# Optimization experiments

Hardware: AMD Instinct MI355X
Metric: run time of the kernel (lower is better)

## Reference

```python
import jax, jax.numpy as jnp
import numpy as np
from jax import lax

WS = 8      # window size (square)
SS = 4      # shift size
HEADS = 8
K = 9       # snake-conv kernel size
CENTER = K // 2
EXT = 1.0   # extend_scope


def _shift_attn_mask(H, W):
    # static numpy construction of Swin shift mask -> [num_windows, L, L]
    m = np.zeros((H, W), dtype=np.float32)
    cnt = 0
    for hs in [(0, -WS), (-WS, -SS), (-SS, None)]:
        for ws_ in [(0, -WS), (-WS, -SS), (-SS, None)]:
            m[hs[0]:hs[1], ws_[0]:ws_[1]] = cnt
            cnt += 1
    m = m.reshape(H // WS, WS, W // WS, WS).transpose(0, 2, 1, 3).reshape(-1, WS * WS)
    d = m[:, None, :] - m[:, :, None]
    return jnp.asarray(np.where(d != 0, -100.0, 0.0).astype(np.float32))


def shifted_window_attention(x, qkv_w, qkv_b, proj_w, proj_b, rel_bias):
    B, H, W, C = x.shape
    d = C // HEADS
    x = jnp.roll(x, shift=(-SS, -SS), axis=(1, 2))
    nH, nW = H // WS, W // WS
    nwin, L = nH * nW, WS * WS
    # window partition -> [B*nwin, L, C]
    xw = x.reshape(B, nH, WS, nW, WS, C).transpose(0, 1, 3, 2, 4, 5).reshape(B * nwin, L, C)
    qkv = (xw @ qkv_w.T + qkv_b).reshape(B * nwin, L, 3, HEADS, d).transpose(2, 0, 3, 1, 4)
    q, k, v = qkv[0] * (d ** -0.5), qkv[1], qkv[2]
    attn = jnp.einsum('nhld,nhmd->nhlm', q, k) + rel_bias[None]
    amask = _shift_attn_mask(H, W)  # [nwin, L, L]
    attn = attn.reshape(B, nwin, HEADS, L, L) + amask[None, :, None]
    attn = jax.nn.softmax(attn.reshape(B * nwin, HEADS, L, L), axis=-1)
    out = jnp.einsum('nhlm,nhmd->nhld', attn, v).transpose(0, 2, 1, 3).reshape(B * nwin, L, C)
    out = out @ proj_w.T + proj_b
    out = out.reshape(B, nH, nW, WS, WS, C).transpose(0, 1, 3, 2, 4, 5).reshape(B, H, W, C)
    return jnp.roll(out, shift=(SS, SS), axis=(1, 2))


def snake_coordinate_map(offset):
    # offset [B, 2K, Wd, Hd], morph=0: cumulative y offsets from the kernel center
    B, _, Wd, Hd = offset.shape
    y_off = offset[:, :K]
    # y_new[center]=0; y_new[center+i]=sum_{j=1..i} y_off[center+j]; mirror below
    up = jnp.cumsum(y_off[:, CENTER + 1:], axis=1)
    down = jnp.cumsum(y_off[:, :CENTER][:, ::-1], axis=1)[:, ::-1]
    y_cum = jnp.concatenate([down, jnp.zeros((B, 1, Wd, Hd), offset.dtype), up], axis=1)
    y_center = jnp.arange(Wd, dtype=offset.dtype)[None, None, :, None]
    y_new = y_center + EXT * y_cum                              # [B,K,Wd,Hd]
    x_spread = jnp.linspace(-CENTER, CENTER, K, dtype=offset.dtype)[None, :, None, None]
    x_center = jnp.arange(Hd, dtype=offset.dtype)[None, None, None, :]
    x_new = jnp.broadcast_to(x_center + x_spread, (B, K, Wd, Hd))
    # rearrange 'b k w h -> b (w k) h'
    y_map = y_new.transpose(0, 2, 1, 3).reshape(B, Wd * K, Hd)
    x_map = x_new.transpose(0, 2, 1, 3).reshape(B, Wd * K, Hd)
    return y_map, x_map


def bilinear_sample(feat, ymap, xmap):
    Hin, Win = feat.shape[-2], feat.shape[-1]
    y = jnp.clip(ymap, 0.0, Hin - 1.0)
    x = jnp.clip(xmap, 0.0, Win - 1.0)
    y0f, x0f = jnp.floor(y), jnp.floor(x)
    wy, wx = y - y0f, x - x0f
    y0 = y0f.astype(jnp.int32); x0 = x0f.astype(jnp.int32)
    y1 = jnp.minimum(y0 + 1, Hin - 1); x1 = jnp.minimum(x0 + 1, Win - 1)
    g = jax.vmap(lambda f, yy, xx: f[:, yy, xx])  # -> [B,C,Ho,Wo]
    v00 = g(feat, y0, x0); v01 = g(feat, y0, x1)
    v10 = g(feat, y1, x0); v11 = g(feat, y1, x1)
    wy = wy[:, None]; wx = wx[:, None]
    return v00 * (1 - wy) * (1 - wx) + v01 * (1 - wy) * wx + v10 * wy * (1 - wx) + v11 * wy * wx


def _forward(x, qkv_weight, qkv_bias, proj_weight, proj_bias, rel_bias, offset, dsc_weight, dsc_bias):
    y = shifted_window_attention(x, qkv_weight, qkv_bias, proj_weight, proj_bias, rel_bias)
    feat = y.transpose(0, 3, 1, 2)                      # NCHW
    ymap, xmap = snake_coordinate_map(offset)
    samp = bilinear_sample(feat, ymap, xmap)            # [B,C,H*K,W]
    out = lax.conv_general_dilated(samp, dsc_weight, window_strides=(K, 1), padding='VALID',
                                   dimension_numbers=('NCHW', 'OIHW', 'NCHW'))
    return jax.nn.relu(out + dsc_bias[None, :, None, None])


def setup_inputs() -> dict:
    key = jax.random.key(0)
    ks = jax.random.split(key, 9)
    B, H, W, C = 8, 64, 64, 256
    return {
        'x': jax.random.normal(ks[0], (B, H, W, C), jnp.float32),
        'qkv_weight': jax.random.normal(ks[1], (3 * C, C), jnp.float32) * 0.05,
        'qkv_bias': jax.random.normal(ks[2], (3 * C,), jnp.float32) * 0.05,
        'proj_weight': jax.random.normal(ks[3], (C, C), jnp.float32) * 0.05,
        'proj_bias': jax.random.normal(ks[4], (C,), jnp.float32) * 0.05,
        'rel_bias': jax.random.normal(ks[5], (HEADS, WS * WS, WS * WS), jnp.float32) * 0.05,
        'offset': jax.random.normal(ks[6], (B, 2 * K, H, W), jnp.float32),
        'dsc_weight': jax.random.normal(ks[7], (C, C, K, 1), jnp.float32) * 0.02,
        'dsc_bias': jax.random.normal(ks[8], (C,), jnp.float32) * 0.02,
    }


def reference(x, qkv_weight, qkv_bias, proj_weight, proj_bias, rel_bias, offset, dsc_weight, dsc_bias):
    return _forward(x, qkv_weight, qkv_bias, proj_weight, proj_bias, rel_bias, offset, dsc_weight, dsc_bias)
```

## Files before the change

### kernel.cpp

```cpp
#include <hip/hip_runtime.h>
#include <math.h>


#define NFLOAT_BUF 8388608

typedef float f32x4 __attribute__((ext_vector_type(4)));
typedef __bf16 bf16x8 __attribute__((ext_vector_type(8)));
typedef _Float16 f16x8 __attribute__((ext_vector_type(8)));

__device__ inline unsigned pack2_bf16(float a, float b) {
    union { float f; unsigned u; } ua, ub;
    ua.f = a; ub.f = b;
    unsigned ra = (ua.u + 0x7FFFu + ((ua.u >> 16) & 1u)) >> 16;
    unsigned rb = (ub.u + 0x7FFFu + ((ub.u >> 16) & 1u)) & 0xFFFF0000u;
    return (ra & 0xFFFFu) | rb;
}
__device__ inline unsigned short pack1_bf16(float a) {
    union { float f; unsigned u; } v;
    v.f = a;
    return (unsigned short)((v.u + 0x7FFFu + ((v.u >> 16) & 1u)) >> 16);
}

__global__ __launch_bounds__(256) void cvt_bf16_kernel(const float* __restrict__ src,
                                                       unsigned short* __restrict__ dst,
                                                       int n8) {
    int t = blockIdx.x * 256 + threadIdx.x;
    if (t >= n8) return;
    const float4* s = (const float4*)(src + (size_t)t * 8);
    float4 a = s[0], b = s[1];
    uint4 o;
    o.x = pack2_bf16(a.x, a.y); o.y = pack2_bf16(a.z, a.w);
    o.z = pack2_bf16(b.x, b.y); o.w = pack2_bf16(b.z, b.w);
    *(uint4*)(dst + (size_t)t * 8) = o;
}

__global__ __launch_bounds__(256) void transpose_w_kernel(const float* __restrict__ w,
                                                          _Float16* __restrict__ wT) {
    int t = blockIdx.x * 256 + threadIdx.x;
    int o = t / 2304;
    int kk = t - o * 2304;
    int k = kk >> 8, i = kk & 255;
    wT[t] = (_Float16)w[(o * 256 + i) * 9 + k];
}

__global__ __launch_bounds__(256) void ymap_kernel(const float* __restrict__ offset,
                                                   float* __restrict__ ymap) {
    int t = blockIdx.x * 256 + threadIdx.x;
    int hd = t & 63;
    int wd = (t >> 6) & 63;
    int b  = t >> 12;
    const float* op = offset + ((size_t)(b * 18) * 64 + wd) * 64 + hd;
    float yo[9];
    #pragma unroll
    for (int k = 0; k < 9; ++k) yo[k] = op[(size_t)k * 4096];
    float cum[9];
    cum[4] = 0.0f;
    float s = 0.0f;
    for (int j = 3; j >= 0; --j) { s += yo[j]; cum[j] = s; }
    s = 0.0f;
    for (int j = 5; j < 9; ++j) { s += yo[j]; cum[j] = s; }
    float wdf = (float)wd;
    float* yp = ymap + ((size_t)(b * 576 + wd * 9)) * 64 + hd;
    #pragma unroll
    for (int k = 0; k < 9; ++k) yp[(size_t)k * 64] = wdf + cum[k];
}

__global__ __launch_bounds__(256) void qkv_mfma_kernel(
    const unsigned short* __restrict__ xb, const unsigned short* __restrict__ wb,
    const float* __restrict__ qkv_b,
    _Float16* __restrict__ qh, _Float16* __restrict__ kh, _Float16* __restrict__ vt) {

    __shared__ __align__(16) char Asb[8192];
    __shared__ __align__(16) char Bsb[32768];
    __shared__ unsigned rowoff[64];

    int nb = blockIdx.x;
    int m0 = blockIdx.y * 64;
    int tid = threadIdx.x;
    int lane = tid & 63, w = tid >> 6;
    int gw = m0 >> 6;

    if (tid < 64) {
        int l = tid;
        int b = gw >> 6, win = gw & 63;
        int rh = ((win >> 3) << 3) + (l >> 3);
        int rw = ((win & 7) << 3) + (l & 7);
        int sh = (rh + 4) & 63, sw = (rw + 4) & 63;
        rowoff[l] = (unsigned)(((b * 64 + sh) * 64 + sw) * 512);
    }

    f32x4 acc[4][4];
    #pragma unroll
    for (int m = 0; m < 4; ++m)
        #pragma unroll
        for (int n = 0; n < 4; ++n) {
            f32x4 z = {0.0f, 0.0f, 0.0f, 0.0f};
            acc[m][n] = z;
        }

    const char* xc = (const char*)xb;
    const char* wc = (const char*)wb;
    int rA = (lane & 15) * 128;
    int u0 = (((lane >> 4)    ) ^ (lane & 7)) << 4;
    int u1 = ((4 + (lane >> 4)) ^ (lane & 7)) << 4;

    __syncthreads();

    for (int c = 0; c < 4; ++c) {
        #pragma unroll
        for (int r = 0; r < 2; ++r) {
            int pos = r * 256 + tid;
            int row = pos >> 3, u = pos & 7;
            const char* src = xc + rowoff[row] + c * 128 + ((u ^ (row & 7)) << 4);
            __builtin_amdgcn_global_load_lds(
                (const __attribute__((address_space(1))) unsigned int*)src,
                (__attribute__((address_space(3))) unsigned int*)(Asb + pos * 16),
                16, 0, 0);
        }
        #pragma unroll
        for (int r = 0; r < 8; ++r) {
            int pos = r * 256 + tid;
            int n = pos >> 3, u = pos & 7;
            const char* src = wc + (size_t)(nb * 256 + n) * 512 + c * 128 + ((u ^ (n & 7)) << 4);
            __builtin_amdgcn_global_load_lds(
                (const __attribute__((address_space(1))) unsigned int*)src,
                (__attribute__((address_space(3))) unsigned int*)(Bsb + pos * 16),
                16, 0, 0);
        }
        __syncthreads();

        bf16x8 av[4][2], bv[4][2];
        #pragma unroll
        for (int m = 0; m < 4; ++m) {
            av[m][0] = *(const bf16x8*)(Asb + m * 2048 + rA + u0);
            av[m][1] = *(const bf16x8*)(Asb + m * 2048 + rA + u1);
        }
        #pragma unroll
        for (int n = 0; n < 4; ++n) {
            bv[n][0] = *(const bf16x8*)(Bsb + w * 8192 + n * 2048 + rA + u0);
            bv[n][1] = *(const bf16x8*)(Bsb + w * 8192 + n * 2048 + rA + u1);
        }
        #pragma unroll
        for (int m = 0; m < 4; ++m)
            #pragma unroll
            for (int n = 0; n < 4; ++n) {
                acc[m][n] = __builtin_amdgcn_mfma_f32_16x16x32_bf16(av[m][0], bv[n][0], acc[m][n], 0, 0, 0);
                acc[m][n] = __builtin_amdgcn_mfma_f32_16x16x32_bf16(av[m][1], bv[n][1], acc[m][n], 0, 0, 0);
            }
        __syncthreads();
    }

    float scale = (nb == 0) ? 0.17677669529663689f : 1.0f;
    #pragma unroll
    for (int nf = 0; nf < 4; ++nf) {
        int o = w * 64 + nf * 16 + (lane & 15);
        float bias = qkv_b[nb * 256 + o];
        int hh = o >> 5, dd = o & 31;
        if (nb < 2) {
            _Float16* dstb = (nb == 0) ? qh : kh;
            _Float16* base = dstb + ((size_t)(gw * 8 + hh) * 64) * 32 + dd;
            #pragma unroll
            for (int mf = 0; mf < 4; ++mf) {
                int l0 = mf * 16 + (lane >> 4) * 4;
                #pragma unroll
                for (int j = 0; j < 4; ++j)
                    base[(size_t)(l0 + j) * 32] = (_Float16)((acc[mf][nf][j] + bias) * scale);
            }
        } else {
            _Float16* base = vt + ((size_t)(gw * 8 + hh) * 32 + dd) * 64;
            #pragma unroll
            for (int mf = 0; mf < 4; ++mf) {
                int l0 = mf * 16 + (lane >> 4) * 4;
                union { _Float16 x[4]; uint2 u; } pk;
                #pragma unroll
                for (int j = 0; j < 4; ++j) pk.x[j] = (_Float16)(acc[mf][nf][j] + bias);
                *(uint2*)(base + l0) = pk.u;
            }
        }
    }
}

__global__ __launch_bounds__(512) void attn_mfma_kernel(
    const _Float16* __restrict__ qh, const _Float16* __restrict__ kh,
    const _Float16* __restrict__ vt, const float* __restrict__ rel_bias,
    unsigned short* __restrict__ attn_ob) {

    __shared__ __align__(16) char Plds[65536];
    int n = blockIdx.x;
    int win = n & 63;
    int wy = win >> 3, wx = win & 7;
    int tid = threadIdx.x, lane = tid & 63, h = tid >> 6;
    int qc = lane & 15, g = lane >> 4;
    char* P = Plds + h * 8192;

    const _Float16* qp = qh + (size_t)(n * 8 + h) * 2048;
    const _Float16* kp = kh + (size_t)(n * 8 + h) * 2048;
    const _Float16* vp = vt + (size_t)(n * 8 + h) * 2048;
    const float* rb = rel_bias + (size_t)h * 4096;

    int rk[16];
    #pragma unroll
    for (int mt = 0; mt < 4; ++mt)
        #pragma unroll
        for (int j = 0; j < 4; ++j) {
            int key = mt * 16 + g * 4 + j;
            int rh = wy * 8 + (key >> 3), rw = wx * 8 + (key & 7);
            rk[mt * 4 + j] = (rh < 56 ? 0 : (rh < 60 ? 1 : 2)) * 3
                           + (rw < 56 ? 0 : (rw < 60 ? 1 : 2));
        }

    f16x8 kf[4];
    #pragma unroll
    for (int mt = 0; mt < 4; ++mt)
        kf[mt] = *(const f16x8*)(kp + (mt * 16 + qc) * 32 + g * 8);

    #pragma unroll
    for (int nt = 0; nt < 4; ++nt) {
        int q = nt * 16 + qc;
        int rqh = wy * 8 + (q >> 3), rqw = wx * 8 + (q & 7);
        int rq = (rqh < 56 ? 0 : (rqh < 60 ? 1 : 2)) * 3
               + (rqw < 56 ? 0 : (rqw < 60 ? 1 : 2));
        f16x8 qf = *(const f16x8*)(qp + q * 32 + g * 8);

        f32x4 s[4];
        #pragma unroll
        for (int mt = 0; mt < 4; ++mt) {
            f32x4 z = {0.0f, 0.0f, 0.0f, 0.0f};
            s[mt] = __builtin_amdgcn_mfma_f32_16x16x32_f16(kf[mt], qf, z, 0, 0, 0);
        }

        float vals[16];
        #pragma unroll
        for (int mt = 0; mt < 4; ++mt) {
            float4 bv4 = *(const float4*)(rb + q * 64 + mt * 16 + g * 4);
            vals[mt * 4 + 0] = s[mt][0] + bv4.x + (rk[mt * 4 + 0] != rq ? -100.0f : 0.0f);
            vals[mt * 4 + 1] = s[mt][1] + bv4.y + (rk[mt * 4 + 1] != rq ? -100.0f : 0.0f);
            vals[mt * 4 + 2] = s[mt][2] + bv4.z + (rk[mt * 4 + 2] != rq ? -100.0f : 0.0f);
            vals[mt * 4 + 3] = s[mt][3] + bv4.w + (rk[mt * 4 + 3] != rq ? -100.0f : 0.0f);
        }

        float mx = vals[0];
        #pragma unroll
        for (int i = 1; i < 16; ++i) mx = fmaxf(mx, vals[i]);
        mx = fmaxf(mx, __shfl_xor(mx, 16));
        mx = fmaxf(mx, __shfl_xor(mx, 32));

        float sum = 0.0f;
        #pragma unroll
        for (int i = 0; i < 16; ++i) { vals[i] = __expf(vals[i] - mx); sum += vals[i]; }
        sum += __shfl_xor(sum, 16);
        sum += __shfl_xor(sum, 32);
        float inv = 1.0f / sum;

        #pragma unroll
        for (int mt = 0; mt < 4; ++mt) {
            union { _Float16 x[4]; uint2 u; } pk4;
            #pragma unroll
            for (int j = 0; j < 4; ++j) pk4.x[j] = (_Float16)(vals[mt * 4 + j] * inv);
            int off = (mt * 32 + g * 8) ^ ((q & 7) << 4);
            *(uint2*)(P + q * 128 + off) = pk4.u;
        }
    }

    f16x8 pa[4][2];
    #pragma unroll
    for (int im = 0; im < 4; ++im)
        #pragma unroll
        for (int ks = 0; ks < 2; ++ks) {
            int row = im * 16 + qc;
            int off = (ks * 64 + g * 16) ^ ((row & 7) << 4);
            pa[im][ks] = *(const f16x8*)(P + row * 128 + off);
        }
    f16x8 bvv[2][2];
    #pragma unroll
    for (int in = 0; in < 2; ++in)
        #pragma unroll
        for (int ks = 0; ks < 2; ++ks)
            bvv[in][ks] = *(const f16x8*)(vp + (in * 16 + qc) * 64 + ks * 32 + g * 8);

    f32x4 acc[4][2];
    #pragma unroll
    for (int im = 0; im < 4; ++im)
        #pragma unroll
        for (int in = 0; in < 2; ++in) {
            f32x4 z = {0.0f, 0.0f, 0.0f, 0.0f};
            acc[im][in] = z;
        }
    #pragma unroll
    for (int im = 0; im < 4; ++im)
        #pragma unroll
        for (int in = 0; in < 2; ++in) {
            acc[im][in] = __builtin_amdgcn_mfma_f32_16x16x32_f16(pa[im][0], bvv[in][0], acc[im][in], 0, 0, 0);
            acc[im][in] = __builtin_amdgcn_mfma_f32_16x16x32_f16(pa[im][1], bvv[in][1], acc[im][in], 0, 0, 0);
        }

    #pragma unroll
    for (int im = 0; im < 4; ++im)
        #pragma unroll
        for (int in = 0; in < 2; ++in)
            #pragma unroll
            for (int j = 0; j < 4; ++j) {
                int q2 = im * 16 + g * 4 + j;
                attn_ob[(size_t)(n * 64 + q2) * 256 + h * 32 + in * 16 + qc] =
                    pack1_bf16(acc[im][in][j]);
            }
}

__global__ __launch_bounds__(256) void proj_mfma_kernel(
    const unsigned short* __restrict__ attn_ob, const unsigned short* __restrict__ pwb,
    const float* __restrict__ proj_b, _Float16* __restrict__ feath) {

    __shared__ __align__(16) char Asb[8192];
    __shared__ __align__(16) char Bsb[32768];

    int m0 = blockIdx.x * 64;
    int tid = threadIdx.x;
    int lane = tid & 63, w = tid >> 6;
    int gw = m0 >> 6;
    int bidx = gw >> 6, win = gw & 63;

    f32x4 acc[4][4];
    #pragma unroll
    for (int m = 0; m < 4; ++m)
        #pragma unroll
        for (int n = 0; n < 4; ++n) {
            f32x4 z = {0.0f, 0.0f, 0.0f, 0.0f};
            acc[m][n] = z;
        }

    const char* ac = (const char*)attn_ob;
    const char* wc = (const char*)pwb;
    int rA = (lane & 15) * 128;
    int u0 = (((lane >> 4)    ) ^ (lane & 7)) << 4;
    int u1 = ((4 + (lane >> 4)) ^ (lane & 7)) << 4;

    for (int c = 0; c < 4; ++c) {
        #pragma unroll
        for (int r = 0; r < 2; ++r) {
            int pos = r * 256 + tid;
            int row = pos >> 3, u = pos & 7;
            const char* src = ac + (size_t)(m0 + row) * 512 + c * 128 + ((u ^ (row & 7)) << 4);
            __builtin_amdgcn_global_load_lds(
                (const __attribute__((address_space(1))) unsigned int*)src,
                (__attribute__((address_space(3))) unsigned int*)(Asb + pos * 16),
                16, 0, 0);
        }
        #pragma unroll
        for (int r = 0; r < 8; ++r) {
            int pos = r * 256 + tid;
            int n = pos >> 3, u = pos & 7;
            const char* src = wc + (size_t)n * 512 + c * 128 + ((u ^ (n & 7)) << 4);
            __builtin_amdgcn_global_load_lds(
                (const __attribute__((address_space(1))) unsigned int*)src,
                (__attribute__((address_space(3))) unsigned int*)(Bsb + pos * 16),
                16, 0, 0);
        }
        __syncthreads();

        bf16x8 av[4][2], bv[4][2];
        #pragma unroll
        for (int m = 0; m < 4; ++m) {
            av[m][0] = *(const bf16x8*)(Asb + m * 2048 + rA + u0);
            av[m][1] = *(const bf16x8*)(Asb + m * 2048 + rA + u1);
        }
        #pragma unroll
        for (int n = 0; n < 4; ++n) {
            bv[n][0] = *(const bf16x8*)(Bsb + w * 8192 + n * 2048 + rA + u0);
            bv[n][1] = *(const bf16x8*)(Bsb + w * 8192 + n * 2048 + rA + u1);
        }
        #pragma unroll
        for (int m = 0; m < 4; ++m)
            #pragma unroll
            for (int n = 0; n < 4; ++n) {
                acc[m][n] = __builtin_amdgcn_mfma_f32_16x16x32_bf16(av[m][0], bv[n][0], acc[m][n], 0, 0, 0);
                acc[m][n] = __builtin_amdgcn_mfma_f32_16x16x32_bf16(av[m][1], bv[n][1], acc[m][n], 0, 0, 0);
            }
        __syncthreads();
    }

    #pragma unroll
    for (int nf = 0; nf < 4; ++nf) {
        int f = w * 64 + nf * 16 + (lane & 15);
        float bias = proj_b[f];
        #pragma unroll
        for (int mf = 0; mf < 4; ++mf) {
            #pragma unroll
            for (int j = 0; j < 4; ++j) {
                int px = mf * 16 + (lane >> 4) * 4 + j;
                int rh = ((win >> 3) << 3) + (px >> 3);
                int rw = ((win & 7) << 3) + (px & 7);
                int p = (rh + 4) & 63;
                int qq = (rw + 4) & 63;
                feath[((size_t)(bidx * 64 + p) * 64 + qq) * 256 + f] =
                    (_Float16)(acc[mf][nf][j] + bias);
            }
        }
    }
}

__global__ __launch_bounds__(256) void sample_conv_mfma2_kernel(
    const _Float16* __restrict__ feath, const float* __restrict__ ymap,
    const _Float16* __restrict__ wT2h, const float* __restrict__ dsc_b,
    float* __restrict__ out) {

    __shared__ __align__(16) char Asb[2][8192];
    __shared__ unsigned row0[9][64];
    __shared__ unsigned row1[9][64];
    __shared__ float    wyv[9][64];

    int blk = blockIdx.x;
    int b = blk & 7, wd = blk >> 3;
    int tid = threadIdx.x;
    int lane = tid & 63, w = tid >> 6;
    int qc = lane & 15, g = lane >> 4;

    for (int idx = tid; idx < 576; idx += 256) {
        int k = idx >> 6, hd = idx & 63;
        float y = ymap[((size_t)(b * 576 + wd * 9 + k)) * 64 + hd];
        y = fminf(fmaxf(y, 0.0f), 63.0f);
        float y0f = floorf(y);
        int y0 = (int)y0f;
        int y1 = min(y0 + 1, 63);
        int xc = min(max(hd + k - 4, 0), 63);
        row0[k][hd] = (unsigned)(((b * 64 + y0) * 64 + xc) * 512);
        row1[k][hd] = (unsigned)(((b * 64 + y1) * 64 + xc) * 512);
        wyv[k][hd] = y - y0f;
    }

    f32x4 acc[4][4];
    #pragma unroll
    for (int m = 0; m < 4; ++m)
        #pragma unroll
        for (int n = 0; n < 4; ++n) {
            f32x4 z = {0.0f, 0.0f, 0.0f, 0.0f};
            acc[m][n] = z;
        }

    const char* featc = (const char*)feath;
    const char* wc    = (const char*)wT2h;

    int pxA0 = tid >> 3;
    int sA   = tid & 7;
    int rA = qc * 128;
    int u0 = ((g    ) ^ (lane & 7)) << 4;
    int u1 = ((4 + g) ^ (lane & 7)) << 4;

    const char* wrow[4];
    #pragma unroll
    for (int n = 0; n < 4; ++n)
        wrow[n] = wc + (size_t)(w * 64 + n * 16 + qc) * 4608 + g * 16;

    f16x8 s0[2], s1[2];
    float swy[2];

    __syncthreads();

    {
        int ks = 0, cib = 0;
        #pragma unroll
        for (int r = 0; r < 2; ++r) {
            int px = pxA0 + r * 32;
            unsigned b0 = row0[ks][px] + cib + sA * 16;
            unsigned b1 = row1[ks][px] + cib + sA * 16;
            swy[r] = wyv[ks][px];
            s0[r] = *(const f16x8*)(featc + b0);
            s1[r] = *(const f16x8*)(featc + b1);
        }
        #pragma unroll
        for (int r = 0; r < 2; ++r) {
            int px = pxA0 + r * 32;
            _Float16 wyh = (_Float16)swy[r];
            _Float16 omh = (_Float16)(1.0f - swy[r]);
            f16x8 res = s0[r] * omh + s1[r] * wyh;
            *(f16x8*)(Asb[0] + px * 128 + ((sA ^ (px & 7)) << 4)) = res;
        }
    }
    __syncthreads();

    for (int c = 0; c < 36; ++c) {
        int cur = c & 1;

        f16x8 bv[4][2];
        #pragma unroll
        for (int n = 0; n < 4; ++n) {
            bv[n][0] = *(const f16x8*)(wrow[n] + c * 128);
            bv[n][1] = *(const f16x8*)(wrow[n] + c * 128 + 64);
        }

        if (c < 35) {
            int cn = c + 1;
            int ks = cn >> 2, cib = (cn & 3) * 128;
            #pragma unroll
            for (int r = 0; r < 2; ++r) {
                int px = pxA0 + r * 32;
                unsigned b0 = row0[ks][px] + cib + sA * 16;
                unsigned b1 = row1[ks][px] + cib + sA * 16;
                swy[r] = wyv[ks][px];
                s0[r] = *(const f16x8*)(featc + b0);
                s1[r] = *(const f16x8*)(featc + b1);
            }
        }

        f16x8 av[4][2];
        #pragma unroll
        for (int m = 0; m < 4; ++m) {
            av[m][0] = *(const f16x8*)(Asb[cur] + m * 2048 + rA + u0);
            av[m][1] = *(const f16x8*)(Asb[cur] + m * 2048 + rA + u1);
        }

        #pragma unroll
        for (int m = 0; m < 4; ++m)
            #pragma unroll
            for (int n = 0; n < 4; ++n) {
                acc[m][n] = __builtin_amdgcn_mfma_f32_16x16x32_f16(av[m][0], bv[n][0], acc[m][n], 0, 0, 0);
                acc[m][n] = __builtin_amdgcn_mfma_f32_16x16x32_f16(av[m][1], bv[n][1], acc[m][n], 0, 0, 0);
            }

        if (c < 35) {
            #pragma unroll
            for (int r = 0; r < 2; ++r) {
                int px = pxA0 + r * 32;
                _Float16 wyh = (_Float16)swy[r];
                _Float16 omh = (_Float16)(1.0f - swy[r]);
                f16x8 res = s0[r] * omh + s1[r] * wyh;
                *(f16x8*)(Asb[cur ^ 1] + px * 128 + ((sA ^ (px & 7)) << 4)) = res;
            }
        }
        __syncthreads();
    }

    #pragma unroll
    for (int n = 0; n < 4; ++n) {
        int o = w * 64 + n * 16 + qc;
        float bvs = dsc_b[o];
        float* orow = out + ((size_t)(b * 256 + o) * 64 + wd) * 64;
        #pragma unroll
        for (int m = 0; m < 4; ++m) {
            int px = m * 16 + g * 4;
            float4 res;
            res.x = fmaxf(acc[m][n][0] + bvs, 0.0f);
            res.y = fmaxf(acc[m][n][1] + bvs, 0.0f);
            res.z = fmaxf(acc[m][n][2] + bvs, 0.0f);
            res.w = fmaxf(acc[m][n][3] + bvs, 0.0f);
            *(float4*)(orow + px) = res;
        }
    }
}

extern "C" void kernel_launch(void* const* d_in, const int* in_sizes, int n_in,
                              void* d_out, int out_size, void* d_ws, size_t ws_size,
                              hipStream_t stream) {
    (void)in_sizes; (void)n_in; (void)out_size; (void)ws_size;
    const float* x        = (const float*)d_in[0];
    const float* qkv_w    = (const float*)d_in[1];
    const float* qkv_b    = (const float*)d_in[2];
    const float* proj_w   = (const float*)d_in[3];
    const float* proj_b   = (const float*)d_in[4];
    const float* rel_bias = (const float*)d_in[5];
    const float* offset   = (const float*)d_in[6];
    const float* dsc_w    = (const float*)d_in[7];
    const float* dsc_b    = (const float*)d_in[8];
    float* out = (float*)d_out;

    unsigned short* wsu = (unsigned short*)d_ws;
    _Float16* qh = (_Float16*)wsu;
    _Float16* kh = (_Float16*)(wsu + NFLOAT_BUF);
    _Float16* vt = (_Float16*)(wsu + 2 * (size_t)NFLOAT_BUF);
    unsigned short* attn_ob = wsu + 3 * (size_t)NFLOAT_BUF;
    _Float16* feath = (_Float16*)(wsu + 4 * (size_t)NFLOAT_BUF);
    unsigned short* xb      = wsu + 5 * (size_t)NFLOAT_BUF;
    unsigned short* wb      = wsu + 6 * (size_t)NFLOAT_BUF;
    unsigned short* pwb     = wb + 196608;
    _Float16* wT2h          = (_Float16*)(pwb + 65536);
    float* ymap = (float*)((unsigned short*)wT2h + 589824);

    cvt_bf16_kernel<<<4096, 256, 0, stream>>>(x, xb, 1048576);
    cvt_bf16_kernel<<<96, 256, 0, stream>>>(qkv_w, wb, 24576);
    cvt_bf16_kernel<<<32, 256, 0, stream>>>(proj_w, pwb, 8192);
    transpose_w_kernel<<<2304, 256, 0, stream>>>(dsc_w, wT2h);
    ymap_kernel<<<128, 256, 0, stream>>>(offset, ymap);
    qkv_mfma_kernel<<<dim3(3, 512), 256, 0, stream>>>(xb, wb, qkv_b, qh, kh, vt);
    attn_mfma_kernel<<<512, 512, 0, stream>>>(qh, kh, vt, rel_bias, attn_ob);
    proj_mfma_kernel<<<512, 256, 0, stream>>>(attn_ob, pwb, proj_b, feath);
    sample_conv_mfma2_kernel<<<512, 256, 0, stream>>>(feath, ymap, wT2h, dsc_b, out);
}
```

Before: 251.6 us.

## Stage conv weights into LDS via direct global-to-LDS loads, drop prefetch pipeline

Replaces per-wave global loads of the conv weight fragments with global_load_lds transfers into a swizzled 32KB shared buffer, read back with the same swizzle as the A tile. The double-buffered A tile with register prefetch of the next chunk is removed; each chunk now gathers A, loads B, syncs, and computes. This targets global load instruction overhead and VGPR pressure for B, at the cost of losing the load/compute overlap and raising shared memory use, which can lower occupancy.

```diff
diff --git a/kernel.cpp b/kernel.cpp
--- a/kernel.cpp
+++ b/kernel.cpp
@@ -398,12 +398,13 @@
     }
 }
 
-__global__ __launch_bounds__(256) void sample_conv_mfma2_kernel(
+__global__ __launch_bounds__(256) void sample_conv_mfma3_kernel(
     const _Float16* __restrict__ feath, const float* __restrict__ ymap,
     const _Float16* __restrict__ wT2h, const float* __restrict__ dsc_b,
     float* __restrict__ out) {
 
-    __shared__ __align__(16) char Asb[2][8192];
+    __shared__ __align__(16) char Asb[8192];
+    __shared__ __align__(16) char Bsb[32768];
     __shared__ unsigned row0[9][64];
     __shared__ unsigned row1[9][64];
     __shared__ float    wyv[9][64];
@@ -445,69 +446,48 @@
     int u0 = ((g    ) ^ (lane & 7)) << 4;
     int u1 = ((4 + g) ^ (lane & 7)) << 4;
 
-    const char* wrow[4];
-    #pragma unroll
-    for (int n = 0; n < 4; ++n)
-        wrow[n] = wc + (size_t)(w * 64 + n * 16 + qc) * 4608 + g * 16;
-
-    f16x8 s0[2], s1[2];
-    float swy[2];
-
     __syncthreads();
 
-    {
-        int ks = 0, cib = 0;
+    for (int c = 0; c < 36; ++c) {
+        #pragma unroll
+        for (int r = 0; r < 8; ++r) {
+            int pos = r * 256 + tid;
+            int n = pos >> 3, uu = pos & 7;
+            int s = uu ^ (n & 7);
+            const char* src = wc + n * 4608 + c * 128 + s * 16;
+            __builtin_amdgcn_global_load_lds(
+                (const __attribute__((address_space(1))) unsigned int*)src,
+                (__attribute__((address_space(3))) unsigned int*)(Bsb + pos * 16),
+                16, 0, 0);
+        }
+        int ks  = c >> 2;
+        int cib = (c & 3) * 128;
         #pragma unroll
         for (int r = 0; r < 2; ++r) {
             int px = pxA0 + r * 32;
             unsigned b0 = row0[ks][px] + cib + sA * 16;
             unsigned b1 = row1[ks][px] + cib + sA * 16;
-            swy[r] = wyv[ks][px];
-            s0[r] = *(const f16x8*)(featc + b0);
-            s1[r] = *(const f16x8*)(featc + b1);
-        }
-        #pragma unroll
-        for (int r = 0; r < 2; ++r) {
-            int px = pxA0 + r * 32;
-            _Float16 wyh = (_Float16)swy[r];
-            _Float16 omh = (_Float16)(1.0f - swy[r]);
-            f16x8 res = s0[r] * omh + s1[r] * wyh;
-            *(f16x8*)(Asb[0] + px * 128 + ((sA ^ (px & 7)) << 4)) = res;
-        }
-    }
-    __syncthreads();
-
-    for (int c = 0; c < 36; ++c) {
-        int cur = c & 1;
-
-        f16x8 bv[4][2];
+            float wy = wyv[ks][px];
+            f16x8 v0 = *(const f16x8*)(featc + b0);
+            f16x8 v1 = *(const f16x8*)(featc + b1);
+            _Float16 wyh = (_Float16)wy;
+            _Float16 omh = (_Float16)(1.0f - wy);
+            f16x8 res = v0 * omh + v1 * wyh;
+            *(f16x8*)(Asb + px * 128 + ((sA ^ (px & 7)) << 4)) = res;
+        }
+        __syncthreads();
+
+        f16x8 av[4][2], bv[4][2];
+        #pragma unroll
+        for (int m = 0; m < 4; ++m) {
+            av[m][0] = *(const f16x8*)(Asb + m * 2048 + rA + u0);
+            av[m][1] = *(const f16x8*)(Asb + m * 2048 + rA + u1);
+        }
         #pragma unroll
         for (int n = 0; n < 4; ++n) {
-            bv[n][0] = *(const f16x8*)(wrow[n] + c * 128);
-            bv[n][1] = *(const f16x8*)(wrow[n] + c * 128 + 64);
-        }
-
-        if (c < 35) {
-            int cn = c + 1;
-            int ks = cn >> 2, cib = (cn & 3) * 128;
-            #pragma unroll
-            for (int r = 0; r < 2; ++r) {
-                int px = pxA0 + r * 32;
-                unsigned b0 = row0[ks][px] + cib + sA * 16;
-                unsigned b1 = row1[ks][px] + cib + sA * 16;
-                swy[r] = wyv[ks][px];
-                s0[r] = *(const f16x8*)(featc + b0);
-                s1[r] = *(const f16x8*)(featc + b1);
-            }
-        }
-
-        f16x8 av[4][2];
-        #pragma unroll
-        for (int m = 0; m < 4; ++m) {
-            av[m][0] = *(const f16x8*)(Asb[cur] + m * 2048 + rA + u0);
-            av[m][1] = *(const f16x8*)(Asb[cur] + m * 2048 + rA + u1);
-        }
-
+            bv[n][0] = *(const f16x8*)(Bsb + w * 8192 + n * 2048 + rA + u0);
+            bv[n][1] = *(const f16x8*)(Bsb + w * 8192 + n * 2048 + rA + u1);
+        }
         #pragma unroll
         for (int m = 0; m < 4; ++m)
             #pragma unroll
@@ -515,17 +495,6 @@
                 acc[m][n] = __builtin_amdgcn_mfma_f32_16x16x32_f16(av[m][0], bv[n][0], acc[m][n], 0, 0, 0);
                 acc[m][n] = __builtin_amdgcn_mfma_f32_16x16x32_f16(av[m][1], bv[n][1], acc[m][n], 0, 0, 0);
             }
-
-        if (c < 35) {
-            #pragma unroll
-            for (int r = 0; r < 2; ++r) {
-                int px = pxA0 + r * 32;
-                _Float16 wyh = (_Float16)swy[r];
-                _Float16 omh = (_Float16)(1.0f - swy[r]);
-                f16x8 res = s0[r] * omh + s1[r] * wyh;
-                *(f16x8*)(Asb[cur ^ 1] + px * 128 + ((sA ^ (px & 7)) << 4)) = res;
-            }
-        }
         __syncthreads();
     }
 
@@ -582,5 +551,5 @@
     qkv_mfma_kernel<<<dim3(3, 512), 256, 0, stream>>>(xb, wb, qkv_b, qh, kh, vt);
     attn_mfma_kernel<<<512, 512, 0, stream>>>(qh, kh, vt, rel_bias, attn_ob);
     proj_mfma_kernel<<<512, 256, 0, stream>>>(attn_ob, pwb, proj_b, feath);
-    sample_conv_mfma2_kernel<<<512, 256, 0, stream>>>(feath, ymap, wT2h, dsc_b, out);
-}
+    sample_conv_mfma3_kernel<<<512, 256, 0, stream>>>(feath, ymap, wT2h, dsc_b, out);
+}
```

New measurement: 227.4 us. -9.6%, faster.
